# Performance work log

Hardware: AMD Instinct MI355X
Metric: run time of the kernel (lower is better)

The kernel has to match this reference:

```python
import jax, jax.numpy as jnp
import numpy as np

B, C, H, W = 64, 2048, 24, 8
NUM_IDS = 751


def setup_inputs() -> dict:
    key = jax.random.key(0)
    k1, k2, k3 = jax.random.split(key, 3)
    features_map = jax.random.normal(k1, (B, C, H, W), dtype=jnp.float32)
    classifier_weight = jax.random.normal(k2, (NUM_IDS, C), dtype=jnp.float32) * 0.02
    pids = jax.random.randint(k3, (B,), 0, NUM_IDS, dtype=jnp.int64)
    return {"features_map": features_map, "classifier_weight": classifier_weight, "pids": pids}


def reference(features_map, classifier_weight, pids):
    b, c, h, w = features_map.shape
    # gather one classifier weight row per sample: [B, C]
    wrows = classifier_weight[pids]
    # per-sample 1xC @ Cx(H*W) matmul -> heatmap [B, H, W]
    heat = jnp.einsum('bc,bchw->bhw', wrows, features_map)
    hflat = heat.reshape(b, h * w)
    mn = hflat.min(axis=-1, keepdims=True)
    mx = hflat.max(axis=-1, keepdims=True)
    # original: normalize only if max != 0
    hflat = jnp.where(mx != 0, (hflat - mn) / (mx - mn), hflat)
    heat = jax.lax.stop_gradient(hflat.reshape(b, h, w))  # heatmap is detached
    return features_map * heat[:, None, :, :]
```

## Files before the change

kernel.cpp:

```cpp
#include <hip/hip_runtime.h>

#define BB 64
#define CC 2048
#define HWN 192
#define HW4 48
#define NCHUNK 16
#define CCHUNK 128
#define TPB 384
#define CLANES 8

#define HEAT_OFF  0
#define CNT_OFF   (BB * HWN)
#define HEATN_OFF (BB * HWN + BB)

__global__ void __launch_bounds__(TPB) heat_atomic_kernel(
    const float* __restrict__ f,
    const float* __restrict__ w,
    const int* __restrict__ pids,
    float* __restrict__ ws)
{
    float* heat  = ws + HEAT_OFF;
    int*   cnt   = (int*)(ws + CNT_OFF);
    float* heatN = ws + HEATN_OFF;

    const int blk = blockIdx.x;
    const int b = blk >> 4;
    const int k = blk & (NCHUNK - 1);
    const int tid = threadIdx.x;
    const int hw4 = tid % HW4;
    const int cl  = tid / HW4;

    __shared__ float wsm[CCHUNK];
    __shared__ __align__(16) float4 red[TPB];
    __shared__ int s_last;
    __shared__ float s_mn, s_mx;

    const int row = pids[b];
    if (tid < CCHUNK) wsm[tid] = w[(size_t)row * CC + (size_t)k * CCHUNK + tid];
    __syncthreads();

    const size_t base = ((size_t)b * CC + (size_t)k * CCHUNK) * HW4;
    const float4* fb4 = (const float4*)f + base;

    float4 acc = make_float4(0.f, 0.f, 0.f, 0.f);
#pragma unroll 8
    for (int c = cl; c < CCHUNK; c += CLANES) {
        float4 v = fb4[(size_t)c * HW4 + hw4];
        float wv = wsm[c];
        acc.x = fmaf(wv, v.x, acc.x);
        acc.y = fmaf(wv, v.y, acc.y);
        acc.z = fmaf(wv, v.z, acc.z);
        acc.w = fmaf(wv, v.w, acc.w);
    }
    red[tid] = acc;
    __syncthreads();
    if (tid < HW4) {
        float4 s = red[tid];
#pragma unroll
        for (int j = 1; j < CLANES; ++j) {
            float4 a = red[tid + j * HW4];
            s.x += a.x; s.y += a.y; s.z += a.z; s.w += a.w;
        }
        float* hp = heat + (size_t)b * HWN + hw4 * 4;
        atomicAdd(hp + 0, s.x);
        atomicAdd(hp + 1, s.y);
        atomicAdd(hp + 2, s.z);
        atomicAdd(hp + 3, s.w);
    }
    __syncthreads();
    if (tid == 0) {
        __threadfence();
        int old = atomicAdd(&cnt[b], 1);
        s_last = (old == NCHUNK - 1);
    }
    __syncthreads();
    if (!s_last) return;

    float v = 0.f;
    if (tid < HWN)
        v = atomicAdd(&heat[(size_t)b * HWN + tid], 0.0f);
    float* vals = (float*)red;
    if (tid < HWN) vals[tid] = v;
    __syncthreads();
    if (tid < 64) {
        float m0 = vals[tid], m1 = vals[tid + 64], m2 = vals[tid + 128];
        float mn = fminf(m0, fminf(m1, m2));
        float mx = fmaxf(m0, fmaxf(m1, m2));
        for (int off = 32; off > 0; off >>= 1) {
            mn = fminf(mn, __shfl_down(mn, off));
            mx = fmaxf(mx, __shfl_down(mx, off));
        }
        if (tid == 0) { s_mn = mn; s_mx = mx; }
    }
    __syncthreads();
    if (tid < HWN) {
        const float mn = s_mn, mx = s_mx;
        heatN[(size_t)b * HWN + tid] = (mx != 0.f) ? (v - mn) / (mx - mn) : v;
    }
}

__global__ void __launch_bounds__(TPB) scale_kernel(
    const float* __restrict__ f,
    const float* __restrict__ ws,
    float* __restrict__ out)
{
    const float* heatN = ws + HEATN_OFF;
    const int blk = blockIdx.x;
    const int b = blk >> 4;
    const int k = blk & (NCHUNK - 1);
    const int tid = threadIdx.x;
    const int hw4 = tid % HW4;
    const int cl  = tid / HW4;

    const float4 hv = ((const float4*)(heatN + (size_t)b * HWN))[hw4];

    const size_t base = ((size_t)b * CC + (size_t)k * CCHUNK) * HW4;
    const float4* fb4 = (const float4*)f + base;
    float4* ob4 = (float4*)out + base;

#pragma unroll 8
    for (int c = cl; c < CCHUNK; c += CLANES) {
        const size_t idx = (size_t)c * HW4 + hw4;
        float4 x = fb4[idx];
        x.x *= hv.x; x.y *= hv.y; x.z *= hv.z; x.w *= hv.w;
        ob4[idx] = x;
    }
}

extern "C" void kernel_launch(void* const* d_in, const int* in_sizes, int n_in,
                              void* d_out, int out_size, void* d_ws, size_t ws_size,
                              hipStream_t stream) {
    const float* features = (const float*)d_in[0];
    const float* weight   = (const float*)d_in[1];
    const int*   pids     = (const int*)d_in[2];
    float* out = (float*)d_out;
    float* ws  = (float*)d_ws;

    hipMemsetAsync(d_ws, 0, (size_t)(BB * HWN + BB) * sizeof(float), stream);

    heat_atomic_kernel<<<BB * NCHUNK, TPB, 0, stream>>>(features, weight, pids, ws);
    scale_kernel<<<BB * NCHUNK, TPB, 0, stream>>>(features, ws, out);
}
```

Baseline: 243.5 us.

## Replace atomic heat accumulation with partial sums and a separate normalize kernel

Each block now writes its per-chunk partial heatmap to workspace instead of using float atomics and a last-block counter. A new small kernel sums the partials per sample and does the min/max normalization. This also removes the memset launch. The scale kernel now uses fully unrolled contiguous indexing with vector-type multiplies and nontemporal stores to avoid polluting cache with output. The cost is an extra kernel launch plus a small partial-buffer round trip.

Result: faster. 197.4 us (-18.9%).

```diff
diff --git a/kernel.cpp b/kernel.cpp
--- a/kernel.cpp
+++ b/kernel.cpp
@@ -9,19 +9,18 @@
 #define TPB 384
 #define CLANES 8
 
-#define HEAT_OFF  0
-#define CNT_OFF   (BB * HWN)
-#define HEATN_OFF (BB * HWN + BB)
+typedef float f32x4 __attribute__((ext_vector_type(4)));
 
-__global__ void __launch_bounds__(TPB) heat_atomic_kernel(
+#define PART_OFF  0
+#define HEATN_OFF (BB * NCHUNK * HWN)
+
+__global__ void __launch_bounds__(TPB) heat_partial_kernel(
     const float* __restrict__ f,
     const float* __restrict__ w,
     const int* __restrict__ pids,
     float* __restrict__ ws)
 {
-    float* heat  = ws + HEAT_OFF;
-    int*   cnt   = (int*)(ws + CNT_OFF);
-    float* heatN = ws + HEATN_OFF;
+    float* partial = ws + PART_OFF;
 
     const int blk = blockIdx.x;
     const int b = blk >> 4;
@@ -32,8 +31,6 @@
 
     __shared__ float wsm[CCHUNK];
     __shared__ __align__(16) float4 red[TPB];
-    __shared__ int s_last;
-    __shared__ float s_mn, s_mx;
 
     const int row = pids[b];
     if (tid < CCHUNK) wsm[tid] = w[(size_t)row * CC + (size_t)k * CCHUNK + tid];
@@ -43,10 +40,10 @@
     const float4* fb4 = (const float4*)f + base;
 
     float4 acc = make_float4(0.f, 0.f, 0.f, 0.f);
-#pragma unroll 8
-    for (int c = cl; c < CCHUNK; c += CLANES) {
-        float4 v = fb4[(size_t)c * HW4 + hw4];
-        float wv = wsm[c];
+#pragma unroll
+    for (int i = 0; i < CCHUNK / CLANES; ++i) {
+        float4 v = fb4[(size_t)i * TPB + tid];
+        float wv = wsm[cl + i * CLANES];
         acc.x = fmaf(wv, v.x, acc.x);
         acc.y = fmaf(wv, v.y, acc.y);
         acc.z = fmaf(wv, v.z, acc.z);
@@ -61,27 +58,29 @@
             float4 a = red[tid + j * HW4];
             s.x += a.x; s.y += a.y; s.z += a.z; s.w += a.w;
         }
-        float* hp = heat + (size_t)b * HWN + hw4 * 4;
-        atomicAdd(hp + 0, s.x);
-        atomicAdd(hp + 1, s.y);
-        atomicAdd(hp + 2, s.z);
-        atomicAdd(hp + 3, s.w);
+        ((float4*)partial)[(size_t)(b * NCHUNK + k) * HW4 + tid] = s;
     }
+}
+
+__global__ void __launch_bounds__(HWN) normalize_kernel(
+    float* __restrict__ ws)
+{
+    const float* partial = ws + PART_OFF;
+    float* heatN = ws + HEATN_OFF;
+
+    const int b = blockIdx.x;
+    const int tid = threadIdx.x;
+
+    __shared__ float vals[HWN];
+    __shared__ float s_mn, s_mx;
+
+    const float* pb = partial + (size_t)b * NCHUNK * HWN + tid;
+    float v = 0.f;
+#pragma unroll
+    for (int kk = 0; kk < NCHUNK; ++kk) v += pb[kk * HWN];
+    vals[tid] = v;
     __syncthreads();
-    if (tid == 0) {
-        __threadfence();
-        int old = atomicAdd(&cnt[b], 1);
-        s_last = (old == NCHUNK - 1);
-    }
-    __syncthreads();
-    if (!s_last) return;
 
-    float v = 0.f;
-    if (tid < HWN)
-        v = atomicAdd(&heat[(size_t)b * HWN + tid], 0.0f);
-    float* vals = (float*)red;
-    if (tid < HWN) vals[tid] = v;
-    __syncthreads();
     if (tid < 64) {
         float m0 = vals[tid], m1 = vals[tid + 64], m2 = vals[tid + 128];
         float mn = fminf(m0, fminf(m1, m2));
@@ -93,10 +92,9 @@
         if (tid == 0) { s_mn = mn; s_mx = mx; }
     }
     __syncthreads();
-    if (tid < HWN) {
-        const float mn = s_mn, mx = s_mx;
-        heatN[(size_t)b * HWN + tid] = (mx != 0.f) ? (v - mn) / (mx - mn) : v;
-    }
+
+    const float mn = s_mn, mx = s_mx;
+    heatN[(size_t)b * HWN + tid] = (mx != 0.f) ? (v - mn) / (mx - mn) : v;
 }
 
 __global__ void __launch_bounds__(TPB) scale_kernel(
@@ -110,20 +108,19 @@
     const int k = blk & (NCHUNK - 1);
     const int tid = threadIdx.x;
     const int hw4 = tid % HW4;
-    const int cl  = tid / HW4;
 
-    const float4 hv = ((const float4*)(heatN + (size_t)b * HWN))[hw4];
+    const f32x4 hv = ((const f32x4*)(heatN + (size_t)b * HWN))[hw4];
 
     const size_t base = ((size_t)b * CC + (size_t)k * CCHUNK) * HW4;
-    const float4* fb4 = (const float4*)f + base;
-    float4* ob4 = (float4*)out + base;
+    const f32x4* fb4 = (const f32x4*)f + base;
+    f32x4* ob4 = (f32x4*)out + base;
 
-#pragma unroll 8
-    for (int c = cl; c < CCHUNK; c += CLANES) {
-        const size_t idx = (size_t)c * HW4 + hw4;
-        float4 x = fb4[idx];
-        x.x *= hv.x; x.y *= hv.y; x.z *= hv.z; x.w *= hv.w;
-        ob4[idx] = x;
+#pragma unroll
+    for (int i = 0; i < (CCHUNK * HW4) / TPB; ++i) {
+        const size_t idx = (size_t)i * TPB + tid;
+        f32x4 x = fb4[idx];
+        x *= hv;
+        __builtin_nontemporal_store(x, &ob4[idx]);
     }
 }
 
@@ -136,8 +133,7 @@
     float* out = (float*)d_out;
     float* ws  = (float*)d_ws;
 
-    hipMemsetAsync(d_ws, 0, (size_t)(BB * HWN + BB) * sizeof(float), stream);
-
-    heat_atomic_kernel<<<BB * NCHUNK, TPB, 0, stream>>>(features, weight, pids, ws);
+    heat_partial_kernel<<<BB * NCHUNK, TPB, 0, stream>>>(features, weight, pids, ws);
+    normalize_kernel<<<BB, HWN, 0, stream>>>(ws);
     scale_kernel<<<BB * NCHUNK, TPB, 0, stream>>>(features, ws, out);
 }
```
